# Performance work log

Measured on AMD Instinct MI355X. Metric: run time of the kernel, lower is better.

Reference implementation:

```python
import jax, jax.numpy as jnp
import numpy as np
from jax import lax

B, T, E, H, V, D_ACT, OUT = 128, 512, 12, 512, 16, 10, 64


def setup_inputs() -> dict:
    key = jax.random.key(0)
    ks = jax.random.split(key, 9)
    ts = jax.random.uniform(ks[0], (B, T, 2), dtype=jnp.float32)
    idx = jax.random.randint(ks[1], (B, T), 0, V).astype(jnp.float32)
    x = jnp.concatenate([ts, idx[..., None]], axis=-1)  # [B,T,3], col2 = activity ids
    emb = jax.random.normal(ks[2], (V, D_ACT), jnp.float32) * 0.1
    emb = emb.at[0].set(0.0)  # padding_idx=0
    W_fwd = jax.random.normal(ks[3], (E, 3 * H), jnp.float32) / np.sqrt(E).astype(np.float32)
    b_fwd = jnp.zeros((3 * H,), jnp.float32)
    W_bwd = jax.random.normal(ks[4], (E, 3 * H), jnp.float32) / np.sqrt(E).astype(np.float32)
    b_bwd = jnp.zeros((3 * H,), jnp.float32)
    weight_Mu = jax.random.normal(ks[5], (2 * H, 1), jnp.float32) * 0.1
    W_out = jax.random.normal(ks[6], (OUT, 2 * H), jnp.float32) * 0.01  # torch Linear layout [out,in]
    b_out = jnp.zeros((OUT,), jnp.float32)
    return {"x": x, "emb": emb, "W_fwd": W_fwd, "b_fwd": b_fwd,
            "W_bwd": W_bwd, "b_bwd": b_bwd, "weight_Mu": weight_Mu,
            "W_out": W_out, "b_out": b_out}


def _fo_pool(z, f):
    # h_t = f_t * h_{t-1} + (1 - f_t) * z_t, scanned over time (axis 0)
    def step(c, zf):
        z_t, f_t = zf
        c = f_t * c + (1.0 - f_t) * z_t
        return c, c
    c0 = jnp.zeros_like(z[0])
    _, cs = lax.scan(step, c0, (z, f))
    return cs  # [T,B,H]


def _qrnn_dir(inp, W, b):
    # inp: [T,B,E] -> gates [T,B,3H]
    Y = inp @ W + b
    Z, F_, O = jnp.split(Y, 3, axis=-1)
    Z = jnp.tanh(Z)
    F_ = jax.nn.sigmoid(F_)
    O = jax.nn.sigmoid(O)
    C = _fo_pool(Z, F_)
    return O * C  # [T,B,H]


def reference(x, emb, W_fwd, b_fwd, W_bwd, b_bwd, weight_Mu, W_out, b_out):
    ts = x[:, :, :2]                                   # [B,T,2] time features
    act = emb[x[:, :, 2].astype(jnp.int32)]            # [B,T,10]
    enc = jnp.concatenate([ts, act], axis=-1)          # [B,T,E]
    inp = jnp.transpose(enc, (1, 0, 2))                # [T,B,E]
    h_f = _qrnn_dir(inp, W_fwd, b_fwd)                 # [T,B,H]
    h_b = _qrnn_dir(inp[::-1], W_bwd, b_bwd)[::-1]     # reverse-direction QRNN
    out = jnp.concatenate([h_f, h_b], axis=-1)         # [T,B,2H]
    out = jax.nn.relu(jnp.transpose(out, (1, 0, 2)))   # [B,T,2H]
    attn = jax.nn.softmax(out @ weight_Mu, axis=1)     # [B,T,1], softmax over time
    context = jnp.einsum('btd,bt->bd', out, attn[..., 0])  # [B,2H]
    context = jax.nn.relu(context)
    return context @ W_out.T + b_out                   # [B,OUT]
```

## Files before the change

kernel.cpp:

```cpp
#include <hip/hip_runtime.h>
#include <hip/hip_bf16.h>

#define B_   128
#define T_   512
#define H_   512
#define V_   16
#define OUT_ 64
#define DH_  1024
#define NCH  16


#define TAB_BYTES (V_*H_*16)
#define TSA_BYTES (T_*8)
#define VPK_BYTES (T_)
#define SCAN_LDS  (TAB_BYTES + TSA_BYTES + VPK_BYTES)

#define LOG2E 1.4426950408889634f

__device__ __forceinline__ float bf2f_lo(unsigned int u) {
    union { unsigned int i; float f; } x; x.i = u << 16; return x.f;
}
__device__ __forceinline__ float bf2f_hi(unsigned int u) {
    union { unsigned int i; float f; } x; x.i = u & 0xffff0000u; return x.f;
}

__device__ __forceinline__ float dot16(const uint4& u0, const uint4& u1,
                                       const float* mu) {
    float s = 0.f;
    s = fmaf(bf2f_lo(u0.x), mu[0],  s); s = fmaf(bf2f_hi(u0.x), mu[1],  s);
    s = fmaf(bf2f_lo(u0.y), mu[2],  s); s = fmaf(bf2f_hi(u0.y), mu[3],  s);
    s = fmaf(bf2f_lo(u0.z), mu[4],  s); s = fmaf(bf2f_hi(u0.z), mu[5],  s);
    s = fmaf(bf2f_lo(u0.w), mu[6],  s); s = fmaf(bf2f_hi(u0.w), mu[7],  s);
    s = fmaf(bf2f_lo(u1.x), mu[8],  s); s = fmaf(bf2f_hi(u1.x), mu[9],  s);
    s = fmaf(bf2f_lo(u1.y), mu[10], s); s = fmaf(bf2f_hi(u1.y), mu[11], s);
    s = fmaf(bf2f_lo(u1.z), mu[12], s); s = fmaf(bf2f_hi(u1.z), mu[13], s);
    s = fmaf(bf2f_lo(u1.w), mu[14], s); s = fmaf(bf2f_hi(u1.w), mu[15], s);
    return s;
}
__device__ __forceinline__ void acc16(const uint4& u0, const uint4& u1,
                                      float e, float* acc) {
    acc[0]  = fmaf(bf2f_lo(u0.x), e, acc[0]);
    acc[1]  = fmaf(bf2f_hi(u0.x), e, acc[1]);
    acc[2]  = fmaf(bf2f_lo(u0.y), e, acc[2]);
    acc[3]  = fmaf(bf2f_hi(u0.y), e, acc[3]);
    acc[4]  = fmaf(bf2f_lo(u0.z), e, acc[4]);
    acc[5]  = fmaf(bf2f_hi(u0.z), e, acc[5]);
    acc[6]  = fmaf(bf2f_lo(u0.w), e, acc[6]);
    acc[7]  = fmaf(bf2f_hi(u0.w), e, acc[7]);
    acc[8]  = fmaf(bf2f_lo(u1.x), e, acc[8]);
    acc[9]  = fmaf(bf2f_hi(u1.x), e, acc[9]);
    acc[10] = fmaf(bf2f_lo(u1.y), e, acc[10]);
    acc[11] = fmaf(bf2f_hi(u1.y), e, acc[11]);
    acc[12] = fmaf(bf2f_lo(u1.z), e, acc[12]);
    acc[13] = fmaf(bf2f_hi(u1.z), e, acc[13]);
    acc[14] = fmaf(bf2f_lo(u1.w), e, acc[14]);
    acc[15] = fmaf(bf2f_hi(u1.w), e, acc[15]);
}

__global__ __launch_bounds__(512) void qrnn_scan12(
    const float* __restrict__ x,
    const float* __restrict__ emb,
    const float* __restrict__ Wf, const float* __restrict__ bf_,
    const float* __restrict__ Wb, const float* __restrict__ bb_,
    __hip_bfloat16* __restrict__ hbuf)
{
    const int b = blockIdx.x, dir = blockIdx.y, h = threadIdx.x;
    const float* __restrict__ W    = dir ? Wb  : Wf;
    const float* __restrict__ bias = dir ? bb_ : bf_;

    extern __shared__ char smem[];
    float4*        tab = (float4*)smem;
    float2*        tsA = (float2*)(smem + TAB_BYTES);
    unsigned char* vpk = (unsigned char*)(smem + TAB_BYTES + TSA_BYTES);

    {
        const int t = h;
        const float* xp = x + ((size_t)b*T_ + t)*3;
        tsA[t] = make_float2(xp[0], xp[1]);
        vpk[t] = (unsigned char)(int)xp[2];
    }

    float w0[3], w1[3], wt[10][3];
#pragma unroll
    for (int g = 0; g < 3; ++g) {
        w0[g] = W[g*H_ + h];
        w1[g] = W[1536 + g*H_ + h];
#pragma unroll
        for (int e = 0; e < 10; ++e)
            wt[e][g] = W[(2+e)*1536 + g*H_ + h];
    }
    const float bz = bias[h], bfv = bias[H_+h], bov = bias[2*H_+h];

    const float FZ = -2.8853900817779268f;
    const float FF = -1.4426950408889634f;

#pragma unroll
    for (int v = 0; v < V_; ++v) {
        float a0 = bz, a1 = bfv, a2 = bov;
#pragma unroll
        for (int e = 0; e < 10; ++e) {
            const float ev = emb[v*10 + e];
            a0 = fmaf(ev, wt[e][0], a0);
            a1 = fmaf(ev, wt[e][1], a1);
            a2 = fmaf(ev, wt[e][2], a2);
        }
        tab[v*H_ + h] = make_float4(FZ*a0, FF*a1, FF*a2, 0.f);
    }
    const float w0z = FZ*w0[0], w0f = FF*w0[1], w0o = FF*w0[2];
    const float w1z = FZ*w1[0], w1f = FF*w1[1], w1o = FF*w1[2];
    __syncthreads();

    const float4* tsA4 = (const float4*)tsA;
    const uint2*  vp2  = (const uint2*)vpk;

    float c = 0.f;
    __hip_bfloat16* hb = hbuf + (size_t)b*T_*DH_ + dir*H_ + h;

#define SS(i, A0, A1, G) { \
    const float zp = fmaf(A0, w0z, fmaf(A1, w1z, (G).x)); \
    const float fp = fmaf(A0, w0f, fmaf(A1, w1f, (G).y)); \
    const float op = fmaf(A0, w0o, fmaf(A1, w1o, (G).z)); \
    const float rz = __builtin_amdgcn_rcpf(1.f + __builtin_amdgcn_exp2f(zp)); \
    const float f  = __builtin_amdgcn_rcpf(1.f + __builtin_amdgcn_exp2f(fp)); \
    const float o  = __builtin_amdgcn_rcpf(1.f + __builtin_amdgcn_exp2f(op)); \
    const float z  = fmaf(2.f, rz, -1.f); \
    c = fmaf(f, c - z, z); \
    const float hv = fmaxf(o * c, 0.f); \
    hb[(size_t)(t0 + (i))*DH_] = __float2bfloat16(hv); \
}

#pragma unroll 2
    for (int gi = 0; gi < T_/8; ++gi) {
        const int gg = dir ? (T_/8 - 1 - gi) : gi;
        const int t0 = gg*8;
        const uint2  vp  = vp2[gg];
        const float4 tsa = tsA4[gg*4 + 0];
        const float4 tsb = tsA4[gg*4 + 1];
        const float4 tsc = tsA4[gg*4 + 2];
        const float4 tsd = tsA4[gg*4 + 3];
        const int v0 =  vp.x        & 255, v1 = (vp.x >> 8) & 255;
        const int v2 = (vp.x >> 16) & 255, v3 =  vp.x >> 24;
        const int v4 =  vp.y        & 255, v5 = (vp.y >> 8) & 255;
        const int v6 = (vp.y >> 16) & 255, v7 =  vp.y >> 24;
        const float4 g0 = tab[v0*H_ + h];
        const float4 g1 = tab[v1*H_ + h];
        const float4 g2 = tab[v2*H_ + h];
        const float4 g3 = tab[v3*H_ + h];
        const float4 g4 = tab[v4*H_ + h];
        const float4 g5 = tab[v5*H_ + h];
        const float4 g6 = tab[v6*H_ + h];
        const float4 g7 = tab[v7*H_ + h];
        if (dir == 0) {
            SS(0, tsa.x, tsa.y, g0) SS(1, tsa.z, tsa.w, g1)
            SS(2, tsb.x, tsb.y, g2) SS(3, tsb.z, tsb.w, g3)
            SS(4, tsc.x, tsc.y, g4) SS(5, tsc.z, tsc.w, g5)
            SS(6, tsd.x, tsd.y, g6) SS(7, tsd.z, tsd.w, g7)
        } else {
            SS(7, tsd.z, tsd.w, g7) SS(6, tsd.x, tsd.y, g6)
            SS(5, tsc.z, tsc.w, g5) SS(4, tsc.x, tsc.y, g4)
            SS(3, tsb.z, tsb.w, g3) SS(2, tsb.x, tsb.y, g2)
            SS(1, tsa.z, tsa.w, g1) SS(0, tsa.x, tsa.y, g0)
        }
    }
#undef SS
}

__global__ __launch_bounds__(256) void postfuse5(
    const __hip_bfloat16* __restrict__ hbuf,
    const float* __restrict__ Mu,
    float* __restrict__ pctx,
    float* __restrict__ pesum)
{
    const int q    = blockIdx.x;
    const int b    = blockIdx.y;
    const int w    = threadIdx.x >> 6;
    const int lane = threadIdx.x & 63;

    __shared__ float pw[4][DH_];
    __shared__ float psum[4];

    float mu[16];
    {
        const float4* mp = (const float4*)Mu;
#pragma unroll
        for (int k = 0; k < 2; ++k) {
            const float4 m0 = mp[(k*64 + lane)*2];
            const float4 m1 = mp[(k*64 + lane)*2 + 1];
            mu[k*8+0]=m0.x; mu[k*8+1]=m0.y; mu[k*8+2]=m0.z; mu[k*8+3]=m0.w;
            mu[k*8+4]=m1.x; mu[k*8+5]=m1.y; mu[k*8+6]=m1.z; mu[k*8+7]=m1.w;
        }
    }

    uint4 U0[8], U1[8];
#pragma unroll
    for (int j = 0; j < 8; ++j) {
        const int t = q*32 + w*8 + j;
        const uint4* hp = (const uint4*)(hbuf + ((size_t)b*T_ + t)*DH_);
        U0[j] = hp[lane];
        U1[j] = hp[64 + lane];
    }

    float sd[8];
#pragma unroll
    for (int j = 0; j < 8; ++j) sd[j] = dot16(U0[j], U1[j], mu);

#pragma unroll
    for (int off = 1; off <= 32; off <<= 1) {
#pragma unroll
        for (int j = 0; j < 8; ++j) sd[j] += __shfl_xor(sd[j], off);
    }

    float e[8];
    float es = 0.f;
#pragma unroll
    for (int j = 0; j < 8; ++j) {
        e[j] = __builtin_amdgcn_exp2f(sd[j] * LOG2E);
        es += e[j];
    }

    float acc[16];
#pragma unroll
    for (int i = 0; i < 16; ++i) acc[i] = 0.f;
#pragma unroll
    for (int j = 0; j < 8; ++j) acc16(U0[j], U1[j], e[j], acc);

#pragma unroll
    for (int k = 0; k < 2; ++k) {
        *(float4*)&pw[w][k*512 + lane*8]     = make_float4(acc[k*8+0], acc[k*8+1], acc[k*8+2], acc[k*8+3]);
        *(float4*)&pw[w][k*512 + lane*8 + 4] = make_float4(acc[k*8+4], acc[k*8+5], acc[k*8+6], acc[k*8+7]);
    }
    if (lane == 0) psum[w] = es;
    __syncthreads();

    float* pc = pctx + ((size_t)b*NCH + q)*DH_;
#pragma unroll
    for (int k = 0; k < 4; ++k) {
        const int d = k*256 + threadIdx.x;
        pc[d] = pw[0][d] + pw[1][d] + pw[2][d] + pw[3][d];
    }
    if (threadIdx.x == 0)
        pesum[b*NCH + q] = psum[0] + psum[1] + psum[2] + psum[3];
}

__global__ __launch_bounds__(512) void combine_out(
    const float* __restrict__ pctx,
    const float* __restrict__ pesum,
    const float* __restrict__ Wout,
    const float* __restrict__ bout,
    float* __restrict__ out)
{
    const int b    = blockIdx.x;
    const int w    = threadIdx.x >> 6;
    const int lane = threadIdx.x & 63;

    __shared__ float ctx[DH_];
    __shared__ float rinv_s;

    {
        const int d = threadIdx.x;
        const float* pc = pctx + (size_t)b*NCH*DH_;
        float c0 = 0.f, c1 = 0.f;
#pragma unroll
        for (int i = 0; i < NCH; ++i) { c0 += pc[i*DH_ + d]; c1 += pc[i*DH_ + d + 512]; }
        ctx[d]       = fmaxf(c0, 0.f);
        ctx[d + 512] = fmaxf(c1, 0.f);
    }
    if (threadIdx.x == 0) {
        float ts = 0.f;
#pragma unroll
        for (int i = 0; i < NCH; ++i) ts += pesum[b*NCH + i];
        rinv_s = __builtin_amdgcn_rcpf(ts);
    }
    __syncthreads();

    const float rinv = rinv_s;
#pragma unroll
    for (int oo = 0; oo < 8; ++oo) {
        const int o = w*8 + oo;
        const float* wp = Wout + o*DH_;
        float a = 0.f;
#pragma unroll
        for (int k = 0; k < 16; ++k) {
            const int d = k*64 + lane;
            a = fmaf(ctx[d], wp[d], a);
        }
#pragma unroll
        for (int off = 1; off <= 32; off <<= 1) a += __shfl_xor(a, off);
        if (lane == 0) out[b*OUT_ + o] = a*rinv + bout[o];
    }
}

extern "C" void kernel_launch(void* const* d_in, const int* in_sizes, int n_in,
                              void* d_out, int out_size, void* d_ws, size_t ws_size,
                              hipStream_t stream)
{
    const float* x    = (const float*)d_in[0];
    const float* emb  = (const float*)d_in[1];
    const float* Wf   = (const float*)d_in[2];
    const float* bf_  = (const float*)d_in[3];
    const float* Wb   = (const float*)d_in[4];
    const float* bb_  = (const float*)d_in[5];
    const float* Mu   = (const float*)d_in[6];
    const float* Wout = (const float*)d_in[7];
    const float* bout = (const float*)d_in[8];
    float* out = (float*)d_out;

    char* ws = (char*)d_ws;
    const size_t hbytes = (size_t)B_*T_*DH_*sizeof(__hip_bfloat16);
    __hip_bfloat16* hbuf = (__hip_bfloat16*)ws;
    float* pctx  = (float*)(ws + hbytes);
    float* pesum = pctx + (size_t)B_*NCH*DH_;

    (void)hipFuncSetAttribute((const void*)qrnn_scan12,
                              hipFuncAttributeMaxDynamicSharedMemorySize,
                              SCAN_LDS);

    qrnn_scan12<<<dim3(B_, 2), 512, SCAN_LDS, stream>>>(x, emb, Wf, bf_, Wb, bb_, hbuf);
    postfuse5<<<dim3(NCH, B_), 256, 0, stream>>>(hbuf, Mu, pctx, pesum);
    combine_out<<<B_, 512, 0, stream>>>(pctx, pesum, Wout, bout, out);
}
```

Before: 170.8 us.

## Stream postfuse rows with a triple-buffered pipeline and halve chunk count

The attention/context reduction kernel now processes 16 time rows per wave with a rolling three-slot register pipeline instead of loading 8 rows up front, and launches half as many chunks per batch (NCH 16 to 8). It adds a launch-bounds occupancy hint. The aim is lower register pressure, higher occupancy, load/compute overlap and less partial-context traffic for combine_out. The trade-off is fewer blocks in flight and a serial shuffle reduction per row.

```diff
diff --git a/kernel.cpp b/kernel.cpp
--- a/kernel.cpp
+++ b/kernel.cpp
@@ -7,7 +7,7 @@
 #define V_   16
 #define OUT_ 64
 #define DH_  1024
-#define NCH  16
+#define NCH  8
 
 
 #define TAB_BYTES (V_*H_*16)
@@ -165,7 +165,7 @@
 #undef SS
 }
 
-__global__ __launch_bounds__(256) void postfuse5(
+__global__ __launch_bounds__(256, 5) void postfuse6(
     const __hip_bfloat16* __restrict__ hbuf,
     const float* __restrict__ Mu,
     float* __restrict__ pctx,
@@ -175,6 +175,7 @@
     const int b    = blockIdx.y;
     const int w    = threadIdx.x >> 6;
     const int lane = threadIdx.x & 63;
+    const int t0   = q*64 + w*16;
 
     __shared__ float pw[4][DH_];
     __shared__ float psum[4];
@@ -191,38 +192,48 @@
         }
     }
 
-    uint4 U0[8], U1[8];
-#pragma unroll
-    for (int j = 0; j < 8; ++j) {
-        const int t = q*32 + w*8 + j;
-        const uint4* hp = (const uint4*)(hbuf + ((size_t)b*T_ + t)*DH_);
-        U0[j] = hp[lane];
-        U1[j] = hp[64 + lane];
-    }
-
-    float sd[8];
-#pragma unroll
-    for (int j = 0; j < 8; ++j) sd[j] = dot16(U0[j], U1[j], mu);
-
-#pragma unroll
-    for (int off = 1; off <= 32; off <<= 1) {
-#pragma unroll
-        for (int j = 0; j < 8; ++j) sd[j] += __shfl_xor(sd[j], off);
-    }
-
-    float e[8];
+    float acc[16];
+#pragma unroll
+    for (int i = 0; i < 16; ++i) acc[i] = 0.f;
     float es = 0.f;
-#pragma unroll
-    for (int j = 0; j < 8; ++j) {
-        e[j] = __builtin_amdgcn_exp2f(sd[j] * LOG2E);
-        es += e[j];
-    }
-
-    float acc[16];
-#pragma unroll
-    for (int i = 0; i < 16; ++i) acc[i] = 0.f;
-#pragma unroll
-    for (int j = 0; j < 8; ++j) acc16(U0[j], U1[j], e[j], acc);
+
+#define LOADROW(j, D0, D1) { \
+    const uint4* hp = (const uint4*)(hbuf + ((size_t)b*T_ + t0 + (j))*DH_); \
+    D0 = hp[lane]; D1 = hp[64 + lane]; }
+
+#define PROCROW(C0, C1) { \
+    float s = dot16(C0, C1, mu); \
+    s += __shfl_xor(s, 1);  s += __shfl_xor(s, 2); \
+    s += __shfl_xor(s, 4);  s += __shfl_xor(s, 8); \
+    s += __shfl_xor(s, 16); s += __shfl_xor(s, 32); \
+    const float e = __builtin_amdgcn_exp2f(s * LOG2E); \
+    es += e; \
+    acc16(C0, C1, e, acc); }
+
+    uint4 A0, A1, B0, B1, C0, C1;
+    LOADROW(0, A0, A1)
+    LOADROW(1, B0, B1)
+    LOADROW(2, C0, C1)
+
+    PROCROW(A0, A1) LOADROW(3,  A0, A1)
+    PROCROW(B0, B1) LOADROW(4,  B0, B1)
+    PROCROW(C0, C1) LOADROW(5,  C0, C1)
+    PROCROW(A0, A1) LOADROW(6,  A0, A1)
+    PROCROW(B0, B1) LOADROW(7,  B0, B1)
+    PROCROW(C0, C1) LOADROW(8,  C0, C1)
+    PROCROW(A0, A1) LOADROW(9,  A0, A1)
+    PROCROW(B0, B1) LOADROW(10, B0, B1)
+    PROCROW(C0, C1) LOADROW(11, C0, C1)
+    PROCROW(A0, A1) LOADROW(12, A0, A1)
+    PROCROW(B0, B1) LOADROW(13, B0, B1)
+    PROCROW(C0, C1) LOADROW(14, C0, C1)
+    PROCROW(A0, A1) LOADROW(15, A0, A1)
+    PROCROW(B0, B1)
+    PROCROW(C0, C1)
+    PROCROW(A0, A1)
+
+#undef LOADROW
+#undef PROCROW
 
 #pragma unroll
     for (int k = 0; k < 2; ++k) {
@@ -316,6 +327,6 @@
                               SCAN_LDS);
 
     qrnn_scan12<<<dim3(B_, 2), 512, SCAN_LDS, stream>>>(x, emb, Wf, bf_, Wb, bb_, hbuf);
-    postfuse5<<<dim3(NCH, B_), 256, 0, stream>>>(hbuf, Mu, pctx, pesum);
+    postfuse6<<<dim3(NCH, B_), 256, 0, stream>>>(hbuf, Mu, pctx, pesum);
     combine_out<<<B_, 512, 0, stream>>>(pctx, pesum, Wout, bout, out);
 }
```

New measurement: 295.6 us. 1.73x slower.
